# Kernel tuning notes

Measured on AMD Instinct MI355X. Metric: run time of the kernel, lower is better.

The kernel has to match this reference:

```python
import jax, jax.numpy as jnp
import numpy as np

K = 5
P = 1.5
MU = 0.01
N_NODES = 100000
N_EDGES = 1600000
D_FEAT = 32


def setup_inputs() -> dict:
    key = jax.random.key(0)
    k1, k2 = jax.random.split(key)
    h = jax.random.normal(k1, (N_NODES, D_FEAT), dtype=jnp.float32)
    edge_index = jax.random.randint(k2, (2, N_EDGES), 0, N_NODES, dtype=jnp.int64)
    return {"h": h, "edge_index": edge_index}


def reference(h, edge_index):
    row, col = edge_index[0], edge_index[1]
    for _ in range(K):
        diff = h[row] - h[col]                      # [E, d] gather
        norm_diff = jnp.maximum(jnp.linalg.norm(diff, axis=1), 1e-6)  # [E]
        weights = (norm_diff / norm_diff.max()) ** (P - 2.0)          # [E]
        # agg[r] += sum over edges with row==r of weights * (h[col] - h[row])
        msgs = weights[:, None] * (-diff)           # [E, d]
        agg = jax.ops.segment_sum(msgs, row, num_segments=N_NODES)    # [N, d]
        h = h - MU * agg
    return h
```

## Files before the change

### kernel.cpp

```cpp
#include <hip/hip_runtime.h>

#define NN 100000
#define NE 1600000
#define DF 32
#define KIT 5
#define MU 0.01f
#define NSLOT 256
#define NV4 (NN * DF / 4)
#define ELLW 36
#define AUXCAP 65536
#define NSLICE 8
#define SLICEN (NN / NSLICE)
#define NSUB 32
#define NBLKA (NE / 256)
#define SEGW 64
#define INVALID_PK 0xffffffffu

typedef float f32x4 __attribute__((ext_vector_type(4)));
typedef float f32x2 __attribute__((ext_vector_type(2)));


__global__ __launch_bounds__(64) void zero_kernel(int* __restrict__ p, int n) {
    int i = blockIdx.x * blockDim.x + threadIdx.x;
    if (i < n) p[i] = 0;
}

__global__ __launch_bounds__(256) void ell_part_kernel(const int* __restrict__ row,
                                                       const int* __restrict__ col,
                                                       unsigned int* __restrict__ buck,
                                                       int* __restrict__ auxcnt,
                                                       int2* __restrict__ aux) {
    __shared__ int wcnt[4][8];
    __shared__ int woff[4][8];
    __shared__ unsigned int sseg[8][SEGW];
    const int t = threadIdx.x;
    const int w = t >> 6;
    const int lane = t & 63;

    ((unsigned int*)sseg)[t] = INVALID_PK;
    ((unsigned int*)sseg)[t + 256] = INVALID_PK;

    const int e = blockIdx.x * 256 + t;
    int b = 8;
    unsigned int packed = INVALID_PK;
    int r = 0, c = 0;
    if (e < NE) {
        r = __builtin_nontemporal_load(&row[e]);
        c = __builtin_nontemporal_load(&col[e]);
        b = r / SLICEN;
        const int rl = r - b * SLICEN;
        packed = ((unsigned int)rl << 17) | (unsigned int)c;
    }

    int myprefix = 0;
    #pragma unroll
    for (int k = 0; k < 8; ++k) {
        const unsigned long long mk = __ballot(b == k);
        if (lane == 0) wcnt[w][k] = __popcll(mk);
        if (k == b) myprefix = __popcll(mk & ((1ull << lane) - 1ull));
    }
    __syncthreads();
    if (t < 32) {
        const int w2 = t >> 3, k = t & 7;
        int o = 0;
        for (int w3 = 0; w3 < w2; ++w3) o += wcnt[w3][k];
        woff[w2][k] = o;
    }
    __syncthreads();

    if (b < 8) {
        const int pos = woff[w][b] + myprefix;
        if (pos < SEGW) {
            sseg[b][pos] = packed;
        } else {
            const int a = atomicAdd(auxcnt, 1);
            if (a < AUXCAP) aux[a] = make_int2(r, c);
        }
    }
    __syncthreads();

    #pragma unroll
    for (int k = 0; k < 2; ++k) {
        const int idx = t + k * 256;
        const int bb = idx >> 6;
        const int j = idx & 63;
        buck[((size_t)bb * NBLKA + blockIdx.x) * SEGW + j] = sseg[bb][j];
    }
}

__global__ __launch_bounds__(1024) void ell_count_kernel(const unsigned int* __restrict__ buck,
                                                         unsigned short* __restrict__ cnt) {
    __shared__ int hist[SLICEN];
    const int t = threadIdx.x;
    const int s = blockIdx.x & (NSLICE - 1);
    const int j = blockIdx.x >> 3;
    const int lane = t & 63;
    const int wid = t >> 6;
    const int blo = j * NBLKA / NSUB;
    const int bhi = (j + 1) * NBLKA / NSUB;

    for (int i = t; i < SLICEN; i += 1024) hist[i] = 0;
    __syncthreads();

    const unsigned int* sp = buck + (size_t)s * NBLKA * SEGW;
    int blk = blo + wid;
    unsigned int pk = (blk < bhi) ? sp[(size_t)blk * SEGW + lane] : INVALID_PK;
    for (; blk < bhi; blk += 16) {
        const int nb = blk + 16;
        const unsigned int nx = (nb < bhi) ? sp[(size_t)nb * SEGW + lane] : INVALID_PK;
        const int rl = (int)(pk >> 17);
        if (rl < SLICEN) atomicAdd(&hist[rl], 1);
        pk = nx;
    }
    __syncthreads();
    unsigned short* cp = cnt + ((size_t)s * NSUB + j) * SLICEN;
    for (int i = t; i < SLICEN; i += 1024) cp[i] = (unsigned short)hist[i];
}

__global__ __launch_bounds__(256) void ell_prefix_kernel(unsigned short* __restrict__ cnt,
                                                         int* __restrict__ degc) {
    const int i = blockIdx.x * blockDim.x + threadIdx.x;
    if (i >= NN) return;
    const int s = i / SLICEN;
    const int rl = i - s * SLICEN;
    unsigned short* cp = cnt + (size_t)s * NSUB * SLICEN + rl;
    int base = 0;
    #pragma unroll
    for (int j = 0; j < NSUB; ++j) {
        const int v = cp[(size_t)j * SLICEN];
        cp[(size_t)j * SLICEN] = (unsigned short)base;
        base += v;
    }
    degc[i] = base;
}

__global__ __launch_bounds__(1024) void ell_place_kernel(const unsigned int* __restrict__ buck,
                                                         const unsigned short* __restrict__ cnt,
                                                         int* __restrict__ colell,
                                                         int* __restrict__ auxcnt,
                                                         int2* __restrict__ aux) {
    __shared__ int cur[SLICEN];
    const int t = threadIdx.x;
    const int s = blockIdx.x & (NSLICE - 1);
    const int j = blockIdx.x >> 3;
    const int lane = t & 63;
    const int wid = t >> 6;
    const int blo = j * NBLKA / NSUB;
    const int bhi = (j + 1) * NBLKA / NSUB;

    const unsigned short* cp = cnt + ((size_t)s * NSUB + j) * SLICEN;
    for (int i = t; i < SLICEN; i += 1024) cur[i] = (int)cp[i];
    __syncthreads();

    const unsigned int* sp = buck + (size_t)s * NBLKA * SEGW;
    int blk = blo + wid;
    unsigned int pk = (blk < bhi) ? sp[(size_t)blk * SEGW + lane] : INVALID_PK;
    for (; blk < bhi; blk += 16) {
        const int nb = blk + 16;
        const unsigned int nx = (nb < bhi) ? sp[(size_t)nb * SEGW + lane] : INVALID_PK;
        const int rl = (int)(pk >> 17);
        if (rl < SLICEN) {
            const int c = (int)(pk & 0x1ffffu);
            const int pos = atomicAdd(&cur[rl], 1);
            const int r = s * SLICEN + rl;
            if (pos < ELLW) {
                colell[r * ELLW + pos] = c;
            } else {
                const int a = atomicAdd(auxcnt, 1);
                if (a < AUXCAP) aux[a] = make_int2(r, c);
            }
        }
        pk = nx;
    }
}


__device__ __forceinline__ unsigned int pack2bf(float a, float b) {
    unsigned int ua = __float_as_uint(a);
    unsigned int ub = __float_as_uint(b);
    return ((ua + 0x8000u) >> 16) | (((ub + 0x8000u) >> 16) << 16);
}

__device__ __forceinline__ f32x2 bf2(unsigned int v) {
    f32x2 r;
    r.x = __uint_as_float(v << 16);
    r.y = __uint_as_float(v & 0xffff0000u);
    return r;
}

__global__ __launch_bounds__(256) void tobf16_kernel(const float* __restrict__ h,
                                                     uint2* __restrict__ hb) {
    int i = blockIdx.x * blockDim.x + threadIdx.x;
    if (i < NV4) {
        const f32x4 v = __builtin_nontemporal_load(((const f32x4*)h) + i);
        hb[i] = make_uint2(pack2bf(v.x, v.y), pack2bf(v.z, v.w));
    }
}


__device__ __forceinline__ void node_head(const uint4* __restrict__ u,
                                          const f32x2* __restrict__ hr2,
                                          f32x2* __restrict__ acc, float& nmax) {
    #pragma unroll
    for (int j = 0; j < 4; ++j) {
        f32x2 d0 = hr2[0] - bf2(u[j].x);
        f32x2 d1 = hr2[1] - bf2(u[j].y);
        f32x2 d2 = hr2[2] - bf2(u[j].z);
        f32x2 d3 = hr2[3] - bf2(u[j].w);
        f32x2 s2 = d0 * d0;
        s2 += d1 * d1;
        s2 += d2 * d2;
        s2 += d3 * d3;
        float s = s2.x + s2.y;
        s += __shfl_xor(s, 1, 32);
        s += __shfl_xor(s, 2, 32);
        const float n = fmaxf(sqrtf(s), 1e-6f);
        nmax = fmaxf(nmax, n);
        const float w = -rsqrtf(n);
        acc[0] += d0 * w;
        acc[1] += d1 * w;
        acc[2] += d2 * w;
        acc[3] += d3 * w;
    }
}

__device__ __forceinline__ void node_tail(const uint4* __restrict__ hb4,
                                          const int* __restrict__ colell, int n,
                                          int deg, int q, int f2,
                                          const f32x2* __restrict__ hr2,
                                          f32x2* __restrict__ acc, float& nmax) {
    for (int k = 32; k < deg; k += 8) {
        const int ei = k + q;
        const int c = (ei < deg) ? colell[n * ELLW + ei] : n;
        const uint4 uu = hb4[c * 4 + f2];
        f32x2 d0 = hr2[0] - bf2(uu.x);
        f32x2 d1 = hr2[1] - bf2(uu.y);
        f32x2 d2 = hr2[2] - bf2(uu.z);
        f32x2 d3 = hr2[3] - bf2(uu.w);
        f32x2 s2 = d0 * d0;
        s2 += d1 * d1;
        s2 += d2 * d2;
        s2 += d3 * d3;
        float s = s2.x + s2.y;
        s += __shfl_xor(s, 1, 32);
        s += __shfl_xor(s, 2, 32);
        const float n2 = fmaxf(sqrtf(s), 1e-6f);
        nmax = fmaxf(nmax, n2);
        const float w = -rsqrtf(n2);
        acc[0] += d0 * w;
        acc[1] += d1 * w;
        acc[2] += d2 * w;
        acc[3] += d3 * w;
    }
}

__global__ __launch_bounds__(256) void agg_kernel(const uint4* __restrict__ hb4,
                                                  const int* __restrict__ degc,
                                                  const int* __restrict__ colell,
                                                  float* __restrict__ S,
                                                  int* __restrict__ maxslots) {
    const int lane = threadIdx.x & 31;
    const int q = lane >> 2;
    const int f2 = lane & 3;
    const int pair = (blockIdx.x * blockDim.x + threadIdx.x) >> 5;
    const int n0 = pair * 2;
    const int n1 = n0 + 1;

    const int d0 = min(degc[n0], ELLW);
    const int d1 = min(degc[n1], ELLW);

    const uint4 hru0 = hb4[n0 * 4 + f2];
    const uint4 hru1 = hb4[n1 * 4 + f2];

    int c0[4], c1[4];
    #pragma unroll
    for (int j = 0; j < 4; ++j) {
        const int e = 8 * j + q;
        c0[j] = (e < d0) ? colell[n0 * ELLW + e] : n0;
        c1[j] = (e < d1) ? colell[n1 * ELLW + e] : n1;
    }

    uint4 u0[4], u1[4];
    #pragma unroll
    for (int j = 0; j < 4; ++j) u0[j] = hb4[c0[j] * 4 + f2];
    #pragma unroll
    for (int j = 0; j < 4; ++j) u1[j] = hb4[c1[j] * 4 + f2];

    f32x2 hr0[4], hr1[4];
    hr0[0] = bf2(hru0.x); hr0[1] = bf2(hru0.y); hr0[2] = bf2(hru0.z); hr0[3] = bf2(hru0.w);
    hr1[0] = bf2(hru1.x); hr1[1] = bf2(hru1.y); hr1[2] = bf2(hru1.z); hr1[3] = bf2(hru1.w);

    f32x2 acc0[4], acc1[4];
    #pragma unroll
    for (int i = 0; i < 4; ++i) {
        acc0[i] = (f32x2){0.0f, 0.0f};
        acc1[i] = (f32x2){0.0f, 0.0f};
    }
    float nmax = 0.0f;

    node_head(u0, hr0, acc0, nmax);
    node_head(u1, hr1, acc1, nmax);

    node_tail(hb4, colell, n0, d0, q, f2, hr0, acc0, nmax);
    node_tail(hb4, colell, n1, d1, q, f2, hr1, acc1, nmax);

    #pragma unroll
    for (int m = 4; m < 32; m <<= 1) {
        #pragma unroll
        for (int i = 0; i < 4; ++i) {
            acc0[i].x += __shfl_xor(acc0[i].x, m, 32);
            acc0[i].y += __shfl_xor(acc0[i].y, m, 32);
            acc1[i].x += __shfl_xor(acc1[i].x, m, 32);
            acc1[i].y += __shfl_xor(acc1[i].y, m, 32);
        }
    }
    if (q == 0) {
        ((float4*)S)[n0 * 8 + f2 * 2] = make_float4(acc0[0].x, acc0[0].y, acc0[1].x, acc0[1].y);
        ((float4*)S)[n0 * 8 + f2 * 2 + 1] = make_float4(acc0[2].x, acc0[2].y, acc0[3].x, acc0[3].y);
        ((float4*)S)[n1 * 8 + f2 * 2] = make_float4(acc1[0].x, acc1[0].y, acc1[1].x, acc1[1].y);
        ((float4*)S)[n1 * 8 + f2 * 2 + 1] = make_float4(acc1[2].x, acc1[2].y, acc1[3].x, acc1[3].y);
    }

    nmax = fmaxf(nmax, __shfl_xor(nmax, 4, 32));
    nmax = fmaxf(nmax, __shfl_xor(nmax, 8, 32));
    nmax = fmaxf(nmax, __shfl_xor(nmax, 16, 32));
    nmax = fmaxf(nmax, __shfl_xor(nmax, 32, 64));
    if ((threadIdx.x & 63) == 0) {
        atomicMax(&maxslots[blockIdx.x & (NSLOT - 1)], __float_as_int(nmax));
    }
}

__global__ __launch_bounds__(256) void aux_kernel(const uint2* __restrict__ hb,
                                                  const int2* __restrict__ aux,
                                                  const int* __restrict__ auxcnt,
                                                  float* __restrict__ S,
                                                  int* __restrict__ maxslots) {
    const int n = min(*auxcnt, AUXCAP);
    for (int i = blockIdx.x * blockDim.x + threadIdx.x; i < n;
         i += gridDim.x * blockDim.x) {
        const int r = aux[i].x;
        const int c = aux[i].y;
        float d[32];
        float s = 0.0f;
        for (int j = 0; j < 8; ++j) {
            const uint2 ur = hb[r * 8 + j];
            const uint2 uc = hb[c * 8 + j];
            float fr[4], fc[4];
            fr[0] = __uint_as_float(ur.x << 16);
            fr[1] = __uint_as_float(ur.x & 0xffff0000u);
            fr[2] = __uint_as_float(ur.y << 16);
            fr[3] = __uint_as_float(ur.y & 0xffff0000u);
            fc[0] = __uint_as_float(uc.x << 16);
            fc[1] = __uint_as_float(uc.x & 0xffff0000u);
            fc[2] = __uint_as_float(uc.y << 16);
            fc[3] = __uint_as_float(uc.y & 0xffff0000u);
            #pragma unroll
            for (int k = 0; k < 4; ++k) {
                d[j * 4 + k] = fr[k] - fc[k];
                s = fmaf(d[j * 4 + k], d[j * 4 + k], s);
            }
        }
        const float nn = fmaxf(sqrtf(s), 1e-6f);
        atomicMax(&maxslots[i & (NSLOT - 1)], __float_as_int(nn));
        const float w = rsqrtf(nn);
        for (int f = 0; f < 32; ++f) atomicAdd(&S[r * DF + f], -d[f] * w);
    }
}

__global__ __launch_bounds__(256) void update_kernel(const float4* __restrict__ hcur,
                                                     float4* __restrict__ hnxt,
                                                     uint2* __restrict__ hb,
                                                     const float4* __restrict__ S,
                                                     const int* __restrict__ slots,
                                                     int writehb) {
    const int t = threadIdx.x;
    int v = slots[t];
    #pragma unroll
    for (int m = 32; m > 0; m >>= 1) v = max(v, __shfl_xor(v, m, 64));
    __shared__ int sm[4];
    __shared__ float sscale;
    if ((t & 63) == 0) sm[t >> 6] = v;
    __syncthreads();
    if (t == 0) {
        int bm = max(max(sm[0], sm[1]), max(sm[2], sm[3]));
        sscale = MU * sqrtf(__int_as_float(bm));
    }
    __syncthreads();
    const float scale = sscale;
    const int i = blockIdx.x * blockDim.x + t;
    if (i < NV4) {
        const float4 hv = hcur[i];
        const float4 sv = S[i];
        float4 o;
        o.x = hv.x - scale * sv.x;
        o.y = hv.y - scale * sv.y;
        o.z = hv.z - scale * sv.z;
        o.w = hv.w - scale * sv.w;
        hnxt[i] = o;
        if (writehb) hb[i] = make_uint2(pack2bf(o.x, o.y), pack2bf(o.z, o.w));
    }
}

extern "C" void kernel_launch(void* const* d_in, const int* in_sizes, int n_in,
                              void* d_out, int out_size, void* d_ws, size_t ws_size,
                              hipStream_t stream) {
    const float* h_in = (const float*)d_in[0];
    const int* row = (const int*)d_in[1];
    const int* col = row + NE;
    float* out = (float*)d_out;

    float* S = (float*)d_ws;
    int* maxslots = (int*)(S + NN * DF);
    int* degc = maxslots + KIT * NSLOT;
    int* auxcnt = degc + NN;
    uintptr_t pa = (uintptr_t)(auxcnt + 1);
    pa = (pa + 7) & ~(uintptr_t)7;
    int2* aux = (int2*)pa;
    int* colell = (int*)(aux + AUXCAP);
    uintptr_t p = (uintptr_t)(colell + NN * ELLW);
    p = (p + 15) & ~(uintptr_t)15;
    uint2* hb = (uint2*)p;
    unsigned int* buck = (unsigned int*)S;
    unsigned short* cnt = (unsigned short*)hb;

    const int fb = NSLICE * NSUB;
    const int pb = (NN + 255) / 256;
    const int gb = (NN / 2 * 32 + 255) / 256;
    const int ub = (NV4 + 255) / 256;

    zero_kernel<<<1, 64, 0, stream>>>(auxcnt, 1);
    ell_part_kernel<<<NBLKA, 256, 0, stream>>>(row, col, buck, auxcnt, aux);
    ell_count_kernel<<<fb, 1024, 0, stream>>>(buck, cnt);
    ell_prefix_kernel<<<pb, 256, 0, stream>>>(cnt, degc);
    ell_place_kernel<<<fb, 1024, 0, stream>>>(buck, cnt, colell, auxcnt, aux);
    tobf16_kernel<<<ub, 256, 0, stream>>>(h_in, hb);

    for (int it = 0; it < KIT; ++it) {
        const float* cur = (it == 0) ? h_in : out;
        agg_kernel<<<gb, 256, 0, stream>>>((const uint4*)hb, degc, colell, S,
                                           maxslots + it * NSLOT);
        aux_kernel<<<32, 256, 0, stream>>>(hb, aux, auxcnt, S, maxslots + it * NSLOT);
        update_kernel<<<ub, 256, 0, stream>>>((const float4*)cur, (float4*)out, hb,
                                              (const float4*)S,
                                              maxslots + it * NSLOT,
                                              (it < KIT - 1) ? 1 : 0);
    }
}
```

Baseline: 373.7 us.

## Fuse overflow-edge aux processing into agg kernel using flagged atomic stores

Removes the separate aux_kernel launch per iteration by running the overflow-edge loop at the end of agg_kernel. Because agg and aux now race on the same S rows, nodes that have overflow edges are flagged in degc. Their S rows are pre-zeroed and their ELL results are added with atomics instead of plain stores, and update_kernel re-zeroes those rows after use. This saves five kernel launches and their serialization. In exchange it adds atomics for flagged nodes and an extra degc read in update.

```diff
diff --git a/kernel.cpp b/kernel.cpp
--- a/kernel.cpp
+++ b/kernel.cpp
@@ -15,6 +15,7 @@
 #define NBLKA (NE / 256)
 #define SEGW 64
 #define INVALID_PK 0xffffffffu
+#define DEGFLAG (1 << 16)
 
 typedef float f32x4 __attribute__((ext_vector_type(4)));
 typedef float f32x2 __attribute__((ext_vector_type(2)));
@@ -189,11 +190,24 @@
 }
 
 __global__ __launch_bounds__(256) void tobf16_kernel(const float* __restrict__ h,
-                                                     uint2* __restrict__ hb) {
+                                                     uint2* __restrict__ hb,
+                                                     const int2* __restrict__ aux,
+                                                     const int* __restrict__ auxcnt,
+                                                     int* __restrict__ degc,
+                                                     float* __restrict__ S) {
     int i = blockIdx.x * blockDim.x + threadIdx.x;
     if (i < NV4) {
         const f32x4 v = __builtin_nontemporal_load(((const f32x4*)h) + i);
         hb[i] = make_uint2(pack2bf(v.x, v.y), pack2bf(v.z, v.w));
+    }
+    const int nA = min(*auxcnt, AUXCAP);
+    for (int a = blockIdx.x * blockDim.x + threadIdx.x; a < nA;
+         a += gridDim.x * blockDim.x) {
+        const int r = aux[a].x;
+        atomicOr(&degc[r], DEGFLAG);
+        f32x4* Sv = (f32x4*)S;
+        #pragma unroll
+        for (int k = 0; k < 8; ++k) Sv[r * 8 + k] = (f32x4){0.f, 0.f, 0.f, 0.f};
     }
 }
 
@@ -254,11 +268,31 @@
     }
 }
 
+__device__ __forceinline__ void store_node(float* __restrict__ S, int n, int f2,
+                                           const f32x2* __restrict__ acc, bool flag) {
+    if (!flag) {
+        ((float4*)S)[n * 8 + f2 * 2] = make_float4(acc[0].x, acc[0].y, acc[1].x, acc[1].y);
+        ((float4*)S)[n * 8 + f2 * 2 + 1] = make_float4(acc[2].x, acc[2].y, acc[3].x, acc[3].y);
+    } else {
+        float* p = S + n * 32 + f2 * 8;
+        atomicAdd(p + 0, acc[0].x);
+        atomicAdd(p + 1, acc[0].y);
+        atomicAdd(p + 2, acc[1].x);
+        atomicAdd(p + 3, acc[1].y);
+        atomicAdd(p + 4, acc[2].x);
+        atomicAdd(p + 5, acc[2].y);
+        atomicAdd(p + 6, acc[3].x);
+        atomicAdd(p + 7, acc[3].y);
+    }
+}
+
 __global__ __launch_bounds__(256) void agg_kernel(const uint4* __restrict__ hb4,
                                                   const int* __restrict__ degc,
                                                   const int* __restrict__ colell,
                                                   float* __restrict__ S,
-                                                  int* __restrict__ maxslots) {
+                                                  int* __restrict__ maxslots,
+                                                  const int2* __restrict__ aux,
+                                                  const int* __restrict__ auxcnt) {
     const int lane = threadIdx.x & 31;
     const int q = lane >> 2;
     const int f2 = lane & 3;
@@ -266,8 +300,10 @@
     const int n0 = pair * 2;
     const int n1 = n0 + 1;
 
-    const int d0 = min(degc[n0], ELLW);
-    const int d1 = min(degc[n1], ELLW);
+    const int v0 = degc[n0];
+    const int v1 = degc[n1];
+    const int d0 = min(v0 & 0xffff, ELLW);
+    const int d1 = min(v1 & 0xffff, ELLW);
 
     const uint4 hru0 = hb4[n0 * 4 + f2];
     const uint4 hru1 = hb4[n1 * 4 + f2];
@@ -315,10 +351,8 @@
         }
     }
     if (q == 0) {
-        ((float4*)S)[n0 * 8 + f2 * 2] = make_float4(acc0[0].x, acc0[0].y, acc0[1].x, acc0[1].y);
-        ((float4*)S)[n0 * 8 + f2 * 2 + 1] = make_float4(acc0[2].x, acc0[2].y, acc0[3].x, acc0[3].y);
-        ((float4*)S)[n1 * 8 + f2 * 2] = make_float4(acc1[0].x, acc1[0].y, acc1[1].x, acc1[1].y);
-        ((float4*)S)[n1 * 8 + f2 * 2 + 1] = make_float4(acc1[2].x, acc1[2].y, acc1[3].x, acc1[3].y);
+        store_node(S, n0, f2, acc0, (v0 & DEGFLAG) != 0);
+        store_node(S, n1, f2, acc1, (v1 & DEGFLAG) != 0);
     }
 
     nmax = fmaxf(nmax, __shfl_xor(nmax, 4, 32));
@@ -328,23 +362,18 @@
     if ((threadIdx.x & 63) == 0) {
         atomicMax(&maxslots[blockIdx.x & (NSLOT - 1)], __float_as_int(nmax));
     }
-}
-
-__global__ __launch_bounds__(256) void aux_kernel(const uint2* __restrict__ hb,
-                                                  const int2* __restrict__ aux,
-                                                  const int* __restrict__ auxcnt,
-                                                  float* __restrict__ S,
-                                                  int* __restrict__ maxslots) {
-    const int n = min(*auxcnt, AUXCAP);
-    for (int i = blockIdx.x * blockDim.x + threadIdx.x; i < n;
+
+    const int nA = min(*auxcnt, AUXCAP);
+    const uint2* hb2 = (const uint2*)hb4;
+    for (int i = blockIdx.x * blockDim.x + threadIdx.x; i < nA;
          i += gridDim.x * blockDim.x) {
         const int r = aux[i].x;
         const int c = aux[i].y;
         float d[32];
         float s = 0.0f;
         for (int j = 0; j < 8; ++j) {
-            const uint2 ur = hb[r * 8 + j];
-            const uint2 uc = hb[c * 8 + j];
+            const uint2 ur = hb2[r * 8 + j];
+            const uint2 uc = hb2[c * 8 + j];
             float fr[4], fc[4];
             fr[0] = __uint_as_float(ur.x << 16);
             fr[1] = __uint_as_float(ur.x & 0xffff0000u);
@@ -370,7 +399,8 @@
 __global__ __launch_bounds__(256) void update_kernel(const float4* __restrict__ hcur,
                                                      float4* __restrict__ hnxt,
                                                      uint2* __restrict__ hb,
-                                                     const float4* __restrict__ S,
+                                                     float* __restrict__ S,
+                                                     const int* __restrict__ degc,
                                                      const int* __restrict__ slots,
                                                      int writehb) {
     const int t = threadIdx.x;
@@ -390,7 +420,7 @@
     const int i = blockIdx.x * blockDim.x + t;
     if (i < NV4) {
         const float4 hv = hcur[i];
-        const float4 sv = S[i];
+        const float4 sv = ((const float4*)S)[i];
         float4 o;
         o.x = hv.x - scale * sv.x;
         o.y = hv.y - scale * sv.y;
@@ -398,6 +428,9 @@
         o.w = hv.w - scale * sv.w;
         hnxt[i] = o;
         if (writehb) hb[i] = make_uint2(pack2bf(o.x, o.y), pack2bf(o.z, o.w));
+        if (degc[i >> 3] & DEGFLAG) {
+            ((float4*)S)[i] = make_float4(0.f, 0.f, 0.f, 0.f);
+        }
     }
 }
 
@@ -433,16 +466,14 @@
     ell_count_kernel<<<fb, 1024, 0, stream>>>(buck, cnt);
     ell_prefix_kernel<<<pb, 256, 0, stream>>>(cnt, degc);
     ell_place_kernel<<<fb, 1024, 0, stream>>>(buck, cnt, colell, auxcnt, aux);
-    tobf16_kernel<<<ub, 256, 0, stream>>>(h_in, hb);
+    tobf16_kernel<<<ub, 256, 0, stream>>>(h_in, hb, aux, auxcnt, degc, S);
 
     for (int it = 0; it < KIT; ++it) {
         const float* cur = (it == 0) ? h_in : out;
         agg_kernel<<<gb, 256, 0, stream>>>((const uint4*)hb, degc, colell, S,
-                                           maxslots + it * NSLOT);
-        aux_kernel<<<32, 256, 0, stream>>>(hb, aux, auxcnt, S, maxslots + it * NSLOT);
+                                           maxslots + it * NSLOT, aux, auxcnt);
         update_kernel<<<ub, 256, 0, stream>>>((const float4*)cur, (float4*)out, hb,
-                                              (const float4*)S,
-                                              maxslots + it * NSLOT,
+                                              S, degc, maxslots + it * NSLOT,
                                               (it < KIT - 1) ? 1 : 0);
     }
 }
```

Result: faster. 364.3 us (-2.5%).
